# Optimization experiments

Hardware: AMD Instinct MI355X
Metric: run time of the kernel (lower is better)

The kernel has to match this reference:

```python
import jax, jax.numpy as jnp
import numpy as np

DIM = 768  # N, feature length and Linear dim
B, C = 16, 1024  # batch, token count


def setup_inputs() -> dict:
    key = jax.random.key(0)
    ks = jax.random.split(key, 7)
    s = 1.0 / np.sqrt(DIM)
    return {
        "x": jax.random.normal(ks[0], (B, C, DIM), dtype=jnp.float32),
        "Wq": jax.random.uniform(ks[1], (DIM, DIM), jnp.float32, -s, s),
        "bq": jax.random.uniform(ks[2], (DIM,), jnp.float32, -s, s),
        "Wk": jax.random.uniform(ks[3], (DIM, DIM), jnp.float32, -s, s),
        "bk": jax.random.uniform(ks[4], (DIM,), jnp.float32, -s, s),
        "Wv": jax.random.uniform(ks[5], (DIM, DIM), jnp.float32, -s, s),
        "bv": jax.random.uniform(ks[6], (DIM,), jnp.float32, -s, s),
    }


def reference(x, Wq, bq, Wk, bk, Wv, bv):
    # x: [B, C, N] with N == DIM; Linears act on last axis (torch y = x W^T + b)
    Bb, Cc, N = x.shape
    q = jnp.einsum("bcn,dn->bcd", x, Wq) + bq
    k = jnp.einsum("bcn,dn->bcd", x, Wk) + bk
    v = jnp.einsum("bcn,dn->bcd", x, Wv) + bv
    attn = jax.nn.softmax(jnp.einsum("bcd,bed->bce", q, k) * (N ** -0.5), axis=-1)  # [B,C,C]
    out = jnp.einsum("bce,ben->bcn", attn, v)  # [B,C,N]
    # faithful to torch: transpose(1,2) then reshape back to (B,C,N) -- a buffer reinterpretation
    out = jnp.transpose(out, (0, 2, 1)).reshape(Bb, Cc, N)
    return out + x  # dropout is identity at inference
```

## Files before the change

kernel.cpp:

```cpp
#include <hip/hip_runtime.h>
#include <hip/hip_bf16.h>

typedef __bf16 v8bf __attribute__((ext_vector_type(8)));
typedef float f32x4 __attribute__((ext_vector_type(4)));

static __device__ __forceinline__ unsigned short f2b(float f){
  union { float f; unsigned int u; } c; c.f = f;
  return (unsigned short)((c.u + 0x7FFFu + ((c.u >> 16) & 1u)) >> 16);
}
static __device__ __forceinline__ float b2f(unsigned int h){
  union { unsigned int u; float f; } c; c.u = h << 16; return c.f;
}

static __device__ __forceinline__ void gld_lds16(const void* g, void* l){
  __builtin_amdgcn_global_load_lds(
      (const __attribute__((address_space(1))) unsigned int*)g,
      (__attribute__((address_space(3))) unsigned int*)l, 16, 0, 0);
}

template<int NW, bool PREF>
static __device__ __forceinline__ void gemm256(
    const unsigned short* __restrict__ A, int lda,
    const unsigned short* __restrict__ B, int ldb,
    int NT, unsigned short* smem, f32x4 acc[8][NW])
{
  const int tid  = threadIdx.x;
  const int lane = tid & 63;
  const int w    = tid >> 6;
  const int wr   = w >> 2, wc = w & 3;
  const int lr   = lane & 15, lg = lane >> 4;
  char* sm = (char*)smem;

  #pragma unroll
  for (int m=0;m<8;++m)
    #pragma unroll
    for (int n=0;n<NW;++n)
      acc[m][n] = (f32x4){0.f,0.f,0.f,0.f};

  const int rloc = tid >> 3;
  const int scol = ((tid & 7) ^ ((tid >> 3) & 7)) << 3;
  const unsigned short* Ab0 = A + (size_t)rloc*lda + scol;
  const unsigned short* Bb0 = B + (size_t)rloc*ldb + scol;

  auto stA = [&](int ds, int i, int kE){
    gld_lds16(Ab0 + (size_t)(i*64)*lda + kE, sm + ds*32768 + i*8192 + w*1024);
  };
  auto stB = [&](int ds, int i, int kE){
    gld_lds16(Bb0 + (size_t)(i*64)*ldb + kE, sm + 65536 + ds*(NW*8192) + i*8192 + w*1024);
  };

  #pragma unroll
  for (int i=0;i<4;++i)  stA(0,i,0);
  #pragma unroll
  for (int i=0;i<NW;++i) stB(0,i,0);
  #pragma unroll
  for (int i=0;i<NW;++i) stB(1,i,64);
  if (NW==4) asm volatile("s_waitcnt vmcnt(4)" ::: "memory");
  else       asm volatile("s_waitcnt vmcnt(3)" ::: "memory");
  __builtin_amdgcn_s_barrier();

  const int ce0 = (((lg*8))      ^ ((lr&7)<<3)) * 2;
  const int ce1 = (((32 + lg*8)) ^ ((lr&7)<<3)) * 2;

  for (int kt = 0; kt < NT; ++kt) {
    const int d  = kt & 1;
    char* Abase = sm + d*32768 + wr*16384;
    char* Bbase = sm + 65536 + d*(NW*8192) + wc*(NW*2048);
    const int kA = (kt+1 < NT ? kt+1 : NT-1)*64;
    const int kB = (kt+2 < NT ? kt+2 : NT-1)*64;
    v8bf bfr[NW][2], af0[2][2], af1[2][2];

    auto rdA = [&](v8bf (&dst)[2][2], int qq){
      #pragma unroll
      for (int mm=0;mm<2;++mm){
        char* rp = Abase + ((qq*2+mm)*16+lr)*128;
        dst[mm][0] = *(const v8bf*)(rp + ce0);
        dst[mm][1] = *(const v8bf*)(rp + ce1);
      }
    };
    auto domfma = [&](v8bf (&cur)[2][2], int qq){
      #pragma unroll
      for (int mm=0;mm<2;++mm)
        #pragma unroll
        for (int n=0;n<NW;++n){
          acc[qq*2+mm][n] = __builtin_amdgcn_mfma_f32_16x16x32_bf16(cur[mm][0], bfr[n][0], acc[qq*2+mm][n], 0,0,0);
          acc[qq*2+mm][n] = __builtin_amdgcn_mfma_f32_16x16x32_bf16(cur[mm][1], bfr[n][1], acc[qq*2+mm][n], 0,0,0);
        }
    };

    #pragma unroll
    for (int q=0;q<4;++q) {
      if (q==0) {
        #pragma unroll
        for (int n=0;n<NW;++n){
          char* rp = Bbase + (n*16+lr)*128;
          bfr[n][0] = *(const v8bf*)(rp + ce0);
          bfr[n][1] = *(const v8bf*)(rp + ce1);
        }
        rdA(af0, 0);
      } else if (!PREF) {
        if ((q&1)==0) rdA(af0, q); else rdA(af1, q);
      }
      if      (q==0){ stA(d^1,0,kA); stA(d^1,1,kA); }
      else if (q==1){ stA(d^1,2,kA); stA(d^1,3,kA); }
      else if (q==2){ stB(d,0,kB);   stB(d,1,kB);   }
      else {
        #pragma unroll
        for (int i=2;i<NW;++i) stB(d,i,kB);
      }
      __builtin_amdgcn_s_barrier();
      asm volatile("s_waitcnt lgkmcnt(0)" ::: "memory");
      __builtin_amdgcn_sched_barrier(0);
      if (PREF && q<3) { if ((q&1)==0) rdA(af1, q+1); else rdA(af0, q+1); }
      __builtin_amdgcn_s_setprio(1);
      if ((q&1)==0) domfma(af0, q); else domfma(af1, q);
      __builtin_amdgcn_s_setprio(0);
      if (q==3){
        if (NW==4) asm volatile("s_waitcnt vmcnt(4)" ::: "memory");
        else       asm volatile("s_waitcnt vmcnt(3)" ::: "memory");
      }
      __builtin_amdgcn_s_barrier();
    }
  }
}

__global__ __launch_bounds__(256) void convert_kernel(
    const float* __restrict__ x,
    const float* __restrict__ Wq, const float* __restrict__ Wk,
    const float* __restrict__ Wv,
    unsigned short* __restrict__ Xb, unsigned short* __restrict__ Wb)
{
  const int NX = 3145728;
  const int NW_ = 147456;
  const int total = NX + 3*NW_;
  for (int i = blockIdx.x*256 + threadIdx.x; i < total; i += gridDim.x*256) {
    const float* src; unsigned short* dst; int off;
    if (i < NX) { src = x; dst = Xb; off = i; }
    else {
      int j = i - NX; int z = j / NW_; off = j - z*NW_;
      src = (z==0) ? Wq : ((z==1) ? Wk : Wv);
      dst = Wb + (size_t)z*589824;
    }
    float4 v = reinterpret_cast<const float4*>(src)[off];
    ushort4 h; h.x=f2b(v.x); h.y=f2b(v.y); h.z=f2b(v.z); h.w=f2b(v.w);
    reinterpret_cast<ushort4*>(dst)[off] = h;
  }
}

__global__ __launch_bounds__(512, 2) void qkv_kernel(
    const unsigned short* __restrict__ Xb, const unsigned short* __restrict__ Wb,
    const float* __restrict__ bq, const float* __restrict__ bk,
    const float* __restrict__ bv,
    unsigned short* __restrict__ Qb, unsigned short* __restrict__ Kb,
    unsigned short* __restrict__ Vt)
{
  extern __shared__ unsigned short smem[];
  const int bid = blockIdx.x;
  const int wg  = (bid & 7)*96 + (bid >> 3);
  const int mt  = wg / 12, nt = wg % 12;

  f32x4 acc[8][3];
  gemm256<3,true>(Xb + (size_t)mt*256*768, 768,
                  Wb + (size_t)nt*192*768, 768, 12, smem, acc);

  const int tid = threadIdx.x, lane = tid & 63, w = tid >> 6;
  const int wr = w >> 2, wc = w & 3, lr = lane & 15, lg = lane >> 4;
  const int z = nt >> 2;
  const float* bias = (z==0) ? bq : ((z==1) ? bk : bv);
  const int colbase = (nt & 3)*192 + wc*48;

  if (z < 2) {
    unsigned short* dst = (z==0) ? Qb : Kb;
    #pragma unroll
    for (int m=0;m<8;++m){
      int row0 = mt*256 + wr*128 + m*16 + lg*4;
      #pragma unroll
      for (int n=0;n<3;++n){
        int col = colbase + n*16 + lr;
        float bb = bias[col];
        #pragma unroll
        for (int r=0;r<4;++r)
          dst[(size_t)(row0+r)*768 + col] = f2b(acc[m][n][r] + bb);
      }
    }
  } else {
    const int rowG0 = mt*256;
    const int batch = rowG0 >> 10;
    const int ebase = rowG0 & 1023;
    unsigned short* dst = Vt + (size_t)batch*786432;
    #pragma unroll
    for (int m=0;m<8;++m){
      int e0 = ebase + wr*128 + m*16 + lg*4;
      #pragma unroll
      for (int n=0;n<3;++n){
        int col = colbase + n*16 + lr;
        float bb = bias[col];
        ushort4 h;
        h.x = f2b(acc[m][n][0] + bb);
        h.y = f2b(acc[m][n][1] + bb);
        h.z = f2b(acc[m][n][2] + bb);
        h.w = f2b(acc[m][n][3] + bb);
        *reinterpret_cast<ushort4*>(dst + (size_t)col*1024 + e0) = h;
      }
    }
  }
}

__global__ __launch_bounds__(512, 2) void scores_kernel(
    const unsigned short* __restrict__ Qb,
    const unsigned short* __restrict__ Kb,
    unsigned short* __restrict__ Sb)
{
  extern __shared__ unsigned short smem[];
  const int mt = blockIdx.x, nt = blockIdx.y, b = blockIdx.z;

  f32x4 acc[8][4];
  gemm256<4,false>(Qb + (size_t)b*786432 + (size_t)mt*256*768, 768,
                   Kb + (size_t)b*786432 + (size_t)nt*256*768, 768, 12, smem, acc);

  const float scale = 0.03608439182435161f;
  const int tid = threadIdx.x, lane = tid & 63, w = tid >> 6;
  const int wr = w >> 2, wc = w & 3, lr = lane & 15, lg = lane >> 4;
  unsigned short* dst = Sb + (size_t)b*1048576;
  #pragma unroll
  for (int m=0;m<8;++m){
    int row0 = mt*256 + wr*128 + m*16 + lg*4;
    #pragma unroll
    for (int n=0;n<4;++n){
      int col = nt*256 + wc*64 + n*16 + lr;
      #pragma unroll
      for (int r=0;r<4;++r)
        dst[(size_t)(row0+r)*1024 + col] = f2b(acc[m][n][r] * scale);
    }
  }
}

__global__ __launch_bounds__(256) void softmax_kernel(unsigned short* __restrict__ S)
{
  int row  = blockIdx.x*4 + (threadIdx.x >> 6);
  int lane = threadIdx.x & 63;
  unsigned short* p = S + (size_t)row*1024 + lane*16;
  uint4 v0 = *reinterpret_cast<const uint4*>(p);
  uint4 v1 = *reinterpret_cast<const uint4*>(p + 8);
  unsigned int uu[8] = {v0.x, v0.y, v0.z, v0.w, v1.x, v1.y, v1.z, v1.w};
  float f[16];
  #pragma unroll
  for (int i=0;i<8;++i){ f[2*i] = b2f(uu[i] & 0xffffu); f[2*i+1] = b2f(uu[i] >> 16); }

  float mx = -1e30f;
  #pragma unroll
  for (int i=0;i<16;++i) mx = fmaxf(mx, f[i]);
  #pragma unroll
  for (int off=1; off<64; off<<=1) mx = fmaxf(mx, __shfl_xor(mx, off, 64));

  float s = 0.f;
  #pragma unroll
  for (int i=0;i<16;++i){ f[i] = __expf(f[i] - mx); s += f[i]; }
  #pragma unroll
  for (int off=1; off<64; off<<=1) s += __shfl_xor(s, off, 64);
  float inv = 1.0f / s;

  #pragma unroll
  for (int i=0;i<8;++i){
    unsigned int lo = f2b(f[2*i] * inv);
    unsigned int hi = f2b(f[2*i+1] * inv);
    uu[i] = lo | (hi << 16);
  }
  uint4 o0; o0.x=uu[0]; o0.y=uu[1]; o0.z=uu[2]; o0.w=uu[3];
  uint4 o1; o1.x=uu[4]; o1.y=uu[5]; o1.z=uu[6]; o1.w=uu[7];
  *reinterpret_cast<uint4*>(p)     = o0;
  *reinterpret_cast<uint4*>(p + 8) = o1;
}

__global__ __launch_bounds__(512, 2) void pv_kernel(
    const unsigned short* __restrict__ P,
    const unsigned short* __restrict__ Vt,
    const float* __restrict__ x, float* __restrict__ out)
{
  extern __shared__ unsigned short smem[];
  const int mt = blockIdx.x, nt = blockIdx.y, b = blockIdx.z;

  f32x4 acc[8][3];
  gemm256<3,true>(P  + (size_t)b*1048576 + (size_t)mt*256*1024, 1024,
                  Vt + (size_t)b*786432  + (size_t)nt*192*1024, 1024, 16, smem, acc);

  const int tid = threadIdx.x, lane = tid & 63, w = tid >> 6;
  const int wr = w >> 2, wc = w & 3, lr = lane & 15, lg = lane >> 4;
  const float* xb = x   + (size_t)b*786432;
  float*       ob = out + (size_t)b*786432;
  #pragma unroll
  for (int m=0;m<8;++m){
    int c0 = mt*256 + wr*128 + m*16 + lg*4;
    #pragma unroll
    for (int n=0;n<3;++n){
      int col = nt*192 + wc*48 + n*16 + lr;
      size_t idx = (size_t)col*1024 + c0;
      float4 xv = *reinterpret_cast<const float4*>(xb + idx);
      float4 o;
      o.x = acc[m][n][0] + xv.x;
      o.y = acc[m][n][1] + xv.y;
      o.z = acc[m][n][2] + xv.z;
      o.w = acc[m][n][3] + xv.w;
      *reinterpret_cast<float4*>(ob + idx) = o;
    }
  }
}

extern "C" void kernel_launch(void* const* d_in, const int* in_sizes, int n_in,
                              void* d_out, int out_size, void* d_ws, size_t ws_size,
                              hipStream_t stream)
{
  const float* x  = (const float*)d_in[0];
  const float* Wq = (const float*)d_in[1];
  const float* bq = (const float*)d_in[2];
  const float* Wk = (const float*)d_in[3];
  const float* bk = (const float*)d_in[4];
  const float* Wv = (const float*)d_in[5];
  const float* bv = (const float*)d_in[6];
  float* out = (float*)d_out;

  char* ws = (char*)d_ws;
  unsigned short* Xb = (unsigned short*)(ws);
  unsigned short* Wb = (unsigned short*)(ws + 25165824);
  unsigned short* Sb = (unsigned short*)(ws);
  unsigned short* Qb = (unsigned short*)(ws + 33554432);
  unsigned short* Kb = (unsigned short*)(ws + 58720256);
  unsigned short* Vt = (unsigned short*)(ws + 83886080);

  convert_kernel<<<dim3(2048),     dim3(256), 0, stream>>>(x, Wq, Wk, Wv, Xb, Wb);
  qkv_kernel    <<<dim3(768),      dim3(512), 114688, stream>>>(Xb, Wb, bq, bk, bv, Qb, Kb, Vt);
  scores_kernel <<<dim3(4, 4, 16), dim3(512), 131072, stream>>>(Qb, Kb, Sb);
  softmax_kernel<<<dim3(4096),     dim3(256), 0, stream>>>(Sb);
  pv_kernel     <<<dim3(4, 4, 16), dim3(512), 114688, stream>>>(Sb, Vt, x, out);
}
```

Measured before the change: 173.1 us.

## Software-pipeline LDS fragment reads across MFMA phases in QKV and PV GEMMs

```diff
diff --git a/kernel.cpp b/kernel.cpp
--- a/kernel.cpp
+++ b/kernel.cpp
@@ -18,8 +18,10 @@
       (__attribute__((address_space(3))) unsigned int*)l, 16, 0, 0);
 }
 
-template<int NW, bool PREF>
-static __device__ __forceinline__ void gemm256(
+#define FENCE __builtin_amdgcn_sched_barrier(0)
+
+template<int NW>
+static __device__ __forceinline__ void gemm256p(
     const unsigned short* __restrict__ A, int lda,
     const unsigned short* __restrict__ B, int ldb,
     int NT, unsigned short* smem, f32x4 acc[8][NW])
@@ -49,14 +51,130 @@
     gld_lds16(Bb0 + (size_t)(i*64)*ldb + kE, sm + 65536 + ds*(NW*8192) + i*8192 + w*1024);
   };
 
+  const int ce0 = (((lg*8))      ^ ((lr&7)<<3)) * 2;
+  const int ce1 = (((32 + lg*8)) ^ ((lr&7)<<3)) * 2;
+
+  v8bf bX[NW][2], bY[NW][2], af0[2][2], af1[2][2];
+
+  auto rdA = [&](v8bf (&dst)[2][2], char* base, int qq){
+    #pragma unroll
+    for (int mm=0;mm<2;++mm){
+      char* rp = base + ((qq*2+mm)*16+lr)*128;
+      dst[mm][0] = *(const v8bf*)(rp + ce0);
+      dst[mm][1] = *(const v8bf*)(rp + ce1);
+    }
+  };
+  auto rdB = [&](v8bf (&dst)[NW][2], char* base){
+    #pragma unroll
+    for (int n=0;n<NW;++n){
+      char* rp = base + (n*16+lr)*128;
+      dst[n][0] = *(const v8bf*)(rp + ce0);
+      dst[n][1] = *(const v8bf*)(rp + ce1);
+    }
+  };
+  auto domfma = [&](v8bf (&a)[2][2], v8bf (&bb)[NW][2], int qq){
+    __builtin_amdgcn_s_setprio(1);
+    #pragma unroll
+    for (int mm=0;mm<2;++mm)
+      #pragma unroll
+      for (int n=0;n<NW;++n){
+        acc[qq*2+mm][n] = __builtin_amdgcn_mfma_f32_16x16x32_bf16(a[mm][0], bb[n][0], acc[qq*2+mm][n], 0,0,0);
+        acc[qq*2+mm][n] = __builtin_amdgcn_mfma_f32_16x16x32_bf16(a[mm][1], bb[n][1], acc[qq*2+mm][n], 0,0,0);
+      }
+    __builtin_amdgcn_s_setprio(0);
+  };
+
+  auto ktile = [&](int kt, int d, v8bf (&bc)[NW][2], v8bf (&bn)[NW][2]){
+    char* Ab = sm + d*32768 + wr*16384;
+    char* An = sm + (d^1)*32768 + wr*16384;
+    char* Bn = sm + 65536 + (d^1)*(NW*8192) + wc*(NW*2048);
+    const int kA = (kt+1 < NT ? kt+1 : NT-1)*64;
+    const int kB = (kt+2 < NT ? kt+2 : NT-1)*64;
+
+    stA(d^1,0,kA); stA(d^1,1,kA);
+    rdA(af1, Ab, 1);
+    FENCE; asm volatile("s_waitcnt lgkmcnt(4)" ::: "memory"); FENCE;
+    domfma(af0, bc, 0);
+    __builtin_amdgcn_s_barrier();
+
+    stA(d^1,2,kA); stA(d^1,3,kA);
+    rdA(af0, Ab, 2);
+    FENCE; asm volatile("s_waitcnt lgkmcnt(4)" ::: "memory"); FENCE;
+    domfma(af1, bc, 1);
+    __builtin_amdgcn_s_barrier();
+
+    stB(d,0,kB); stB(d,1,kB);
+    rdA(af1, Ab, 3);
+    FENCE; asm volatile("s_waitcnt lgkmcnt(4)" ::: "memory"); FENCE;
+    domfma(af0, bc, 2);
+    asm volatile("s_waitcnt vmcnt(2)" ::: "memory");
+    __builtin_amdgcn_s_barrier();
+
+    #pragma unroll
+    for (int i=2;i<NW;++i) stB(d,i,kB);
+    rdA(af0, An, 0);
+    rdB(bn, Bn);
+    if (NW==3) { FENCE; asm volatile("s_waitcnt lgkmcnt(10)" ::: "memory"); FENCE; }
+    else       { FENCE; asm volatile("s_waitcnt lgkmcnt(12)" ::: "memory"); FENCE; }
+    domfma(af1, bc, 3);
+    __builtin_amdgcn_s_barrier();
+  };
+
   #pragma unroll
   for (int i=0;i<4;++i)  stA(0,i,0);
   #pragma unroll
   for (int i=0;i<NW;++i) stB(0,i,0);
   #pragma unroll
   for (int i=0;i<NW;++i) stB(1,i,64);
-  if (NW==4) asm volatile("s_waitcnt vmcnt(4)" ::: "memory");
-  else       asm volatile("s_waitcnt vmcnt(3)" ::: "memory");
+  if (NW==3) asm volatile("s_waitcnt vmcnt(3)" ::: "memory");
+  else       asm volatile("s_waitcnt vmcnt(4)" ::: "memory");
+  __builtin_amdgcn_s_barrier();
+  rdB(bX, sm + 65536 + wc*(NW*2048));
+  rdA(af0, sm + wr*16384, 0);
+
+  for (int kt = 0; kt < NT; kt += 2) {
+    ktile(kt,   0, bX, bY);
+    ktile(kt+1, 1, bY, bX);
+  }
+}
+
+static __device__ __forceinline__ void gemm256v1(
+    const unsigned short* __restrict__ A, int lda,
+    const unsigned short* __restrict__ B, int ldb,
+    int NT, unsigned short* smem, f32x4 acc[8][4])
+{
+  const int tid  = threadIdx.x;
+  const int lane = tid & 63;
+  const int w    = tid >> 6;
+  const int wr   = w >> 2, wc = w & 3;
+  const int lr   = lane & 15, lg = lane >> 4;
+  char* sm = (char*)smem;
+
+  #pragma unroll
+  for (int m=0;m<8;++m)
+    #pragma unroll
+    for (int n=0;n<4;++n)
+      acc[m][n] = (f32x4){0.f,0.f,0.f,0.f};
+
+  const int rloc = tid >> 3;
+  const int scol = ((tid & 7) ^ ((tid >> 3) & 7)) << 3;
+  const unsigned short* Ab0 = A + (size_t)rloc*lda + scol;
+  const unsigned short* Bb0 = B + (size_t)rloc*ldb + scol;
+
+  auto stA = [&](int ds, int i, int kE){
+    gld_lds16(Ab0 + (size_t)(i*64)*lda + kE, sm + ds*32768 + i*8192 + w*1024);
+  };
+  auto stB = [&](int ds, int i, int kE){
+    gld_lds16(Bb0 + (size_t)(i*64)*ldb + kE, sm + 65536 + ds*32768 + i*8192 + w*1024);
+  };
+
+  #pragma unroll
+  for (int i=0;i<4;++i) stA(0,i,0);
+  #pragma unroll
+  for (int i=0;i<4;++i) stB(0,i,0);
+  #pragma unroll
+  for (int i=0;i<4;++i) stB(1,i,64);
+  asm volatile("s_waitcnt vmcnt(4)" ::: "memory");
   __builtin_amdgcn_s_barrier();
 
   const int ce0 = (((lg*8))      ^ ((lr&7)<<3)) * 2;
@@ -65,10 +183,10 @@
   for (int kt = 0; kt < NT; ++kt) {
     const int d  = kt & 1;
     char* Abase = sm + d*32768 + wr*16384;
-    char* Bbase = sm + 65536 + d*(NW*8192) + wc*(NW*2048);
+    char* Bbase = sm + 65536 + d*32768 + wc*8192;
     const int kA = (kt+1 < NT ? kt+1 : NT-1)*64;
     const int kB = (kt+2 < NT ? kt+2 : NT-1)*64;
-    v8bf bfr[NW][2], af0[2][2], af1[2][2];
+    v8bf bfr[4][2], af0[2][2], af1[2][2];
 
     auto rdA = [&](v8bf (&dst)[2][2], int qq){
       #pragma unroll
@@ -82,7 +200,7 @@
       #pragma unroll
       for (int mm=0;mm<2;++mm)
         #pragma unroll
-        for (int n=0;n<NW;++n){
+        for (int n=0;n<4;++n){
           acc[qq*2+mm][n] = __builtin_amdgcn_mfma_f32_16x16x32_bf16(cur[mm][0], bfr[n][0], acc[qq*2+mm][n], 0,0,0);
           acc[qq*2+mm][n] = __builtin_amdgcn_mfma_f32_16x16x32_bf16(cur[mm][1], bfr[n][1], acc[qq*2+mm][n], 0,0,0);
         }
@@ -92,33 +210,26 @@
     for (int q=0;q<4;++q) {
       if (q==0) {
         #pragma unroll
-        for (int n=0;n<NW;++n){
+        for (int n=0;n<4;++n){
           char* rp = Bbase + (n*16+lr)*128;
           bfr[n][0] = *(const v8bf*)(rp + ce0);
           bfr[n][1] = *(const v8bf*)(rp + ce1);
         }
         rdA(af0, 0);
-      } else if (!PREF) {
+      } else {
         if ((q&1)==0) rdA(af0, q); else rdA(af1, q);
       }
       if      (q==0){ stA(d^1,0,kA); stA(d^1,1,kA); }
       else if (q==1){ stA(d^1,2,kA); stA(d^1,3,kA); }
       else if (q==2){ stB(d,0,kB);   stB(d,1,kB);   }
-      else {
-        #pragma unroll
-        for (int i=2;i<NW;++i) stB(d,i,kB);
-      }
+      else          { stB(d,2,kB);   stB(d,3,kB);   }
       __builtin_amdgcn_s_barrier();
       asm volatile("s_waitcnt lgkmcnt(0)" ::: "memory");
-      __builtin_amdgcn_sched_barrier(0);
-      if (PREF && q<3) { if ((q&1)==0) rdA(af1, q+1); else rdA(af0, q+1); }
+      FENCE;
       __builtin_amdgcn_s_setprio(1);
       if ((q&1)==0) domfma(af0, q); else domfma(af1, q);
       __builtin_amdgcn_s_setprio(0);
-      if (q==3){
-        if (NW==4) asm volatile("s_waitcnt vmcnt(4)" ::: "memory");
-        else       asm volatile("s_waitcnt vmcnt(3)" ::: "memory");
-      }
+      if (q==3) asm volatile("s_waitcnt vmcnt(4)" ::: "memory");
       __builtin_amdgcn_s_barrier();
     }
   }
@@ -160,8 +271,8 @@
   const int mt  = wg / 12, nt = wg % 12;
 
   f32x4 acc[8][3];
-  gemm256<3,true>(Xb + (size_t)mt*256*768, 768,
-                  Wb + (size_t)nt*192*768, 768, 12, smem, acc);
+  gemm256p<3>(Xb + (size_t)mt*256*768, 768,
+              Wb + (size_t)nt*192*768, 768, 12, smem, acc);
 
   const int tid = threadIdx.x, lane = tid & 63, w = tid >> 6;
   const int wr = w >> 2, wc = w & 3, lr = lane & 15, lg = lane >> 4;
@@ -215,8 +326,8 @@
   const int mt = blockIdx.x, nt = blockIdx.y, b = blockIdx.z;
 
   f32x4 acc[8][4];
-  gemm256<4,false>(Qb + (size_t)b*786432 + (size_t)mt*256*768, 768,
-                   Kb + (size_t)b*786432 + (size_t)nt*256*768, 768, 12, smem, acc);
+  gemm256v1(Qb + (size_t)b*786432 + (size_t)mt*256*768, 768,
+            Kb + (size_t)b*786432 + (size_t)nt*256*768, 768, 12, smem, acc);
 
   const float scale = 0.03608439182435161f;
   const int tid = threadIdx.x, lane = tid & 63, w = tid >> 6;
@@ -281,8 +392,8 @@
   const int mt = blockIdx.x, nt = blockIdx.y, b = blockIdx.z;
 
   f32x4 acc[8][3];
-  gemm256<3,true>(P  + (size_t)b*1048576 + (size_t)mt*256*1024, 1024,
-                  Vt + (size_t)b*786432  + (size_t)nt*192*1024, 1024, 16, smem, acc);
+  gemm256p<3>(P  + (size_t)b*1048576 + (size_t)mt*256*1024, 1024,
+              Vt + (size_t)b*786432  + (size_t)nt*192*1024, 1024, 16, smem, acc);
 
   const int tid = threadIdx.x, lane = tid & 63, w = tid >> 6;
   const int wr = w >> 2, wc = w & 3, lr = lane & 15, lg = lane >> 4;
```

Measured after the change: 165.1 us. -4.6%, faster.

## Fold softmax into score epilogue and PV normalization, deepen GEMM pipelining

Applied to the files above, without the earlier changes.

```diff
diff --git a/kernel.cpp b/kernel.cpp
--- a/kernel.cpp
+++ b/kernel.cpp
@@ -10,6 +10,13 @@
 }
 static __device__ __forceinline__ float b2f(unsigned int h){
   union { unsigned int u; float f; } c; c.u = h << 16; return c.f;
+}
+static __device__ __forceinline__ float sum8(v8bf v){
+  union { v8bf v; unsigned int u[4]; } c; c.v = v;
+  float s = 0.f;
+  #pragma unroll
+  for (int i=0;i<4;++i){ s += b2f(c.u[i] & 0xffffu); s += b2f(c.u[i] >> 16); }
+  return s;
 }
 
 static __device__ __forceinline__ void gld_lds16(const void* g, void* l){
@@ -18,11 +25,13 @@
       (__attribute__((address_space(3))) unsigned int*)l, 16, 0, 0);
 }
 
-template<int NW, bool PREF>
-static __device__ __forceinline__ void gemm256(
+#define FENCE __builtin_amdgcn_sched_barrier(0)
+
+template<int NW, bool DEEP, bool RS>
+static __device__ __forceinline__ void gemmcore(
     const unsigned short* __restrict__ A, int lda,
     const unsigned short* __restrict__ B, int ldb,
-    int NT, unsigned short* smem, f32x4 acc[8][NW])
+    int NT, unsigned short* smem, f32x4 acc[8][NW], float* rs)
 {
   const int tid  = threadIdx.x;
   const int lane = tid & 63;
@@ -30,96 +39,139 @@
   const int wr   = w >> 2, wc = w & 3;
   const int lr   = lane & 15, lg = lane >> 4;
   char* sm = (char*)smem;
+  constexpr int NAB   = DEEP ? 3 : 2;
+  constexpr int BBASE = NAB * 32768;
+  constexpr int BBUF  = NW * 8192;
 
   #pragma unroll
   for (int m=0;m<8;++m)
     #pragma unroll
     for (int n=0;n<NW;++n)
       acc[m][n] = (f32x4){0.f,0.f,0.f,0.f};
+  if (RS) {
+    #pragma unroll
+    for (int m=0;m<8;++m) rs[m] = 0.f;
+  }
 
   const int rloc = tid >> 3;
   const int scol = ((tid & 7) ^ ((tid >> 3) & 7)) << 3;
   const unsigned short* Ab0 = A + (size_t)rloc*lda + scol;
   const unsigned short* Bb0 = B + (size_t)rloc*ldb + scol;
 
-  auto stA = [&](int ds, int i, int kE){
-    gld_lds16(Ab0 + (size_t)(i*64)*lda + kE, sm + ds*32768 + i*8192 + w*1024);
-  };
-  auto stB = [&](int ds, int i, int kE){
-    gld_lds16(Bb0 + (size_t)(i*64)*ldb + kE, sm + 65536 + ds*(NW*8192) + i*8192 + w*1024);
-  };
-
-  #pragma unroll
-  for (int i=0;i<4;++i)  stA(0,i,0);
-  #pragma unroll
-  for (int i=0;i<NW;++i) stB(0,i,0);
-  #pragma unroll
-  for (int i=0;i<NW;++i) stB(1,i,64);
-  if (NW==4) asm volatile("s_waitcnt vmcnt(4)" ::: "memory");
-  else       asm volatile("s_waitcnt vmcnt(3)" ::: "memory");
-  __builtin_amdgcn_s_barrier();
+  auto stA = [&](int ab, int i, int kE){
+    gld_lds16(Ab0 + (size_t)(i*64)*lda + kE, sm + ab*32768 + i*8192 + w*1024);
+  };
+  auto stB = [&](int db, int i, int kE){
+    gld_lds16(Bb0 + (size_t)(i*64)*ldb + kE, sm + BBASE + db*BBUF + i*8192 + w*1024);
+  };
 
   const int ce0 = (((lg*8))      ^ ((lr&7)<<3)) * 2;
   const int ce1 = (((32 + lg*8)) ^ ((lr&7)<<3)) * 2;
 
-  for (int kt = 0; kt < NT; ++kt) {
-    const int d  = kt & 1;
-    char* Abase = sm + d*32768 + wr*16384;
-    char* Bbase = sm + 65536 + d*(NW*8192) + wc*(NW*2048);
-    const int kA = (kt+1 < NT ? kt+1 : NT-1)*64;
+  v8bf bX[NW][2], bY[NW][2], af0[2][2], af1[2][2];
+
+  auto rdA = [&](v8bf (&dst)[2][2], char* base, int qq){
+    #pragma unroll
+    for (int mm=0;mm<2;++mm){
+      char* rp = base + ((qq*2+mm)*16+lr)*128;
+      dst[mm][0] = *(const v8bf*)(rp + ce0);
+      dst[mm][1] = *(const v8bf*)(rp + ce1);
+    }
+  };
+  auto rdB = [&](v8bf (&dst)[NW][2], char* base){
+    #pragma unroll
+    for (int n=0;n<NW;++n){
+      char* rp = base + (n*16+lr)*128;
+      dst[n][0] = *(const v8bf*)(rp + ce0);
+      dst[n][1] = *(const v8bf*)(rp + ce1);
+    }
+  };
+  auto domfma = [&](v8bf (&a)[2][2], v8bf (&bb)[NW][2], int qq){
+    __builtin_amdgcn_s_setprio(1);
+    #pragma unroll
+    for (int mm=0;mm<2;++mm)
+      #pragma unroll
+      for (int n=0;n<NW;++n){
+        acc[qq*2+mm][n] = __builtin_amdgcn_mfma_f32_16x16x32_bf16(a[mm][0], bb[n][0], acc[qq*2+mm][n], 0,0,0);
+        acc[qq*2+mm][n] = __builtin_amdgcn_mfma_f32_16x16x32_bf16(a[mm][1], bb[n][1], acc[qq*2+mm][n], 0,0,0);
+      }
+    __builtin_amdgcn_s_setprio(0);
+    if (RS){
+      rs[qq*2]   += sum8(a[0][0]) + sum8(a[0][1]);
+      rs[qq*2+1] += sum8(a[1][0]) + sum8(a[1][1]);
+    }
+  };
+
+  auto ktile = [&](int kt, int ar, int an, int as,
+                   v8bf (&bc)[NW][2], v8bf (&bn)[NW][2]){
+    char* Ab = sm + ar*32768 + wr*16384;
+    char* An = sm + an*32768 + wr*16384;
+    char* Bn = sm + BBASE + ((kt+1)&1)*BBUF + wc*(NW*2048);
+    const int kAraw = DEEP ? kt+2 : kt+1;
+    const int kA = (kAraw < NT ? kAraw : NT-1)*64;
     const int kB = (kt+2 < NT ? kt+2 : NT-1)*64;
-    v8bf bfr[NW][2], af0[2][2], af1[2][2];
-
-    auto rdA = [&](v8bf (&dst)[2][2], int qq){
-      #pragma unroll
-      for (int mm=0;mm<2;++mm){
-        char* rp = Abase + ((qq*2+mm)*16+lr)*128;
-        dst[mm][0] = *(const v8bf*)(rp + ce0);
-        dst[mm][1] = *(const v8bf*)(rp + ce1);
-      }
-    };
-    auto domfma = [&](v8bf (&cur)[2][2], int qq){
-      #pragma unroll
-      for (int mm=0;mm<2;++mm)
-        #pragma unroll
-        for (int n=0;n<NW;++n){
-          acc[qq*2+mm][n] = __builtin_amdgcn_mfma_f32_16x16x32_bf16(cur[mm][0], bfr[n][0], acc[qq*2+mm][n], 0,0,0);
-          acc[qq*2+mm][n] = __builtin_amdgcn_mfma_f32_16x16x32_bf16(cur[mm][1], bfr[n][1], acc[qq*2+mm][n], 0,0,0);
-        }
-    };
-
-    #pragma unroll
-    for (int q=0;q<4;++q) {
-      if (q==0) {
-        #pragma unroll
-        for (int n=0;n<NW;++n){
-          char* rp = Bbase + (n*16+lr)*128;
-          bfr[n][0] = *(const v8bf*)(rp + ce0);
-          bfr[n][1] = *(const v8bf*)(rp + ce1);
-        }
-        rdA(af0, 0);
-      } else if (!PREF) {
-        if ((q&1)==0) rdA(af0, q); else rdA(af1, q);
-      }
-      if      (q==0){ stA(d^1,0,kA); stA(d^1,1,kA); }
-      else if (q==1){ stA(d^1,2,kA); stA(d^1,3,kA); }
-      else if (q==2){ stB(d,0,kB);   stB(d,1,kB);   }
-      else {
-        #pragma unroll
-        for (int i=2;i<NW;++i) stB(d,i,kB);
-      }
-      __builtin_amdgcn_s_barrier();
-      asm volatile("s_waitcnt lgkmcnt(0)" ::: "memory");
-      __builtin_amdgcn_sched_barrier(0);
-      if (PREF && q<3) { if ((q&1)==0) rdA(af1, q+1); else rdA(af0, q+1); }
-      __builtin_amdgcn_s_setprio(1);
-      if ((q&1)==0) domfma(af0, q); else domfma(af1, q);
-      __builtin_amdgcn_s_setprio(0);
-      if (q==3){
-        if (NW==4) asm volatile("s_waitcnt vmcnt(4)" ::: "memory");
-        else       asm volatile("s_waitcnt vmcnt(3)" ::: "memory");
-      }
-      __builtin_amdgcn_s_barrier();
+    const int db = kt & 1;
+
+    stA(as,0,kA); stA(as,1,kA);
+    rdA(af1, Ab, 1);
+    FENCE; asm volatile("s_waitcnt lgkmcnt(4)" ::: "memory"); FENCE;
+    domfma(af0, bc, 0);
+    __builtin_amdgcn_s_barrier();
+
+    stA(as,2,kA); stA(as,3,kA);
+    rdA(af0, Ab, 2);
+    FENCE; asm volatile("s_waitcnt lgkmcnt(4)" ::: "memory"); FENCE;
+    domfma(af1, bc, 1);
+    __builtin_amdgcn_s_barrier();
+
+    stB(db,0,kB); stB(db,1,kB);
+    rdA(af1, Ab, 3);
+    FENCE; asm volatile("s_waitcnt lgkmcnt(4)" ::: "memory"); FENCE;
+    domfma(af0, bc, 2);
+    if constexpr (DEEP) asm volatile("s_waitcnt vmcnt(6)" ::: "memory");
+    else                asm volatile("s_waitcnt vmcnt(2)" ::: "memory");
+    __builtin_amdgcn_s_barrier();
+
+    #pragma unroll
+    for (int i=2;i<NW;++i) stB(db,i,kB);
+    rdA(af0, An, 0);
+    rdB(bn, Bn);
+    if constexpr (NW==3) { FENCE; asm volatile("s_waitcnt lgkmcnt(10)" ::: "memory"); FENCE; }
+    else                 { FENCE; asm volatile("s_waitcnt lgkmcnt(12)" ::: "memory"); FENCE; }
+    domfma(af1, bc, 3);
+    __builtin_amdgcn_s_barrier();
+  };
+
+  #pragma unroll
+  for (int i=0;i<4;++i)  stA(0,i,0);
+  #pragma unroll
+  for (int i=0;i<NW;++i) stB(0,i,0);
+  if constexpr (DEEP) {
+    #pragma unroll
+    for (int i=0;i<4;++i) stA(1,i,64);
+  }
+  #pragma unroll
+  for (int i=0;i<NW;++i) stB(1,i,64);
+  if constexpr (DEEP)      asm volatile("s_waitcnt vmcnt(7)" ::: "memory");
+  else if constexpr (NW==3) asm volatile("s_waitcnt vmcnt(3)" ::: "memory");
+  else                      asm volatile("s_waitcnt vmcnt(4)" ::: "memory");
+  __builtin_amdgcn_s_barrier();
+  rdB(bX, sm + BBASE + wc*(NW*2048));
+  rdA(af0, sm + wr*16384, 0);
+
+  if constexpr (DEEP) {
+    int c0 = 0;
+    for (int kt = 0; kt < NT; kt += 2) {
+      const int c1 = (c0+1==3) ? 0 : c0+1;
+      const int c2 = (c1+1==3) ? 0 : c1+1;
+      ktile(kt,   c0, c1, c2, bX, bY);
+      ktile(kt+1, c1, c2, c0, bY, bX);
+      c0 = c2;
+    }
+  } else {
+    for (int kt = 0; kt < NT; kt += 2) {
+      ktile(kt,   0, 1, 1, bX, bY);
+      ktile(kt+1, 1, 0, 0, bY, bX);
     }
   }
 }
@@ -160,8 +212,8 @@
   const int mt  = wg / 12, nt = wg % 12;
 
   f32x4 acc[8][3];
-  gemm256<3,true>(Xb + (size_t)mt*256*768, 768,
-                  Wb + (size_t)nt*192*768, 768, 12, smem, acc);
+  gemmcore<3,true,false>(Xb + (size_t)mt*256*768, 768,
+                         Wb + (size_t)nt*192*768, 768, 12, smem, acc, nullptr);
 
   const int tid = threadIdx.x, lane = tid & 63, w = tid >> 6;
   const int wr = w >> 2, wc = w & 3, lr = lane & 15, lg = lane >> 4;
@@ -209,19 +261,20 @@
 __global__ __launch_bounds__(512, 2) void scores_kernel(
     const unsigned short* __restrict__ Qb,
     const unsigned short* __restrict__ Kb,
-    unsigned short* __restrict__ Sb)
+    unsigned short* __restrict__ Eb)
 {
   extern __shared__ unsigned short smem[];
   const int mt = blockIdx.x, nt = blockIdx.y, b = blockIdx.z;
 
   f32x4 acc[8][4];
-  gemm256<4,false>(Qb + (size_t)b*786432 + (size_t)mt*256*768, 768,
-                   Kb + (size_t)b*786432 + (size_t)nt*256*768, 768, 12, smem, acc);
+  gemmcore<4,false,false>(Qb + (size_t)b*786432 + (size_t)mt*256*768, 768,
+                          Kb + (size_t)b*786432 + (size_t)nt*256*768, 768,
+                          12, smem, acc, nullptr);
 
   const float scale = 0.03608439182435161f;
   const int tid = threadIdx.x, lane = tid & 63, w = tid >> 6;
   const int wr = w >> 2, wc = w & 3, lr = lane & 15, lg = lane >> 4;
-  unsigned short* dst = Sb + (size_t)b*1048576;
+  unsigned short* dst = Eb + (size_t)b*1048576;
   #pragma unroll
   for (int m=0;m<8;++m){
     int row0 = mt*256 + wr*128 + m*16 + lg*4;
@@ -230,50 +283,13 @@
       int col = nt*256 + wc*64 + n*16 + lr;
       #pragma unroll
       for (int r=0;r<4;++r)
-        dst[(size_t)(row0+r)*1024 + col] = f2b(acc[m][n][r] * scale);
-    }
-  }
-}
-
-__global__ __launch_bounds__(256) void softmax_kernel(unsigned short* __restrict__ S)
-{
-  int row  = blockIdx.x*4 + (threadIdx.x >> 6);
-  int lane = threadIdx.x & 63;
-  unsigned short* p = S + (size_t)row*1024 + lane*16;
-  uint4 v0 = *reinterpret_cast<const uint4*>(p);
-  uint4 v1 = *reinterpret_cast<const uint4*>(p + 8);
-  unsigned int uu[8] = {v0.x, v0.y, v0.z, v0.w, v1.x, v1.y, v1.z, v1.w};
-  float f[16];
-  #pragma unroll
-  for (int i=0;i<8;++i){ f[2*i] = b2f(uu[i] & 0xffffu); f[2*i+1] = b2f(uu[i] >> 16); }
-
-  float mx = -1e30f;
-  #pragma unroll
-  for (int i=0;i<16;++i) mx = fmaxf(mx, f[i]);
-  #pragma unroll
-  for (int off=1; off<64; off<<=1) mx = fmaxf(mx, __shfl_xor(mx, off, 64));
-
-  float s = 0.f;
-  #pragma unroll
-  for (int i=0;i<16;++i){ f[i] = __expf(f[i] - mx); s += f[i]; }
-  #pragma unroll
-  for (int off=1; off<64; off<<=1) s += __shfl_xor(s, off, 64);
-  float inv = 1.0f / s;
-
-  #pragma unroll
-  for (int i=0;i<8;++i){
-    unsigned int lo = f2b(f[2*i] * inv);
-    unsigned int hi = f2b(f[2*i+1] * inv);
-    uu[i] = lo | (hi << 16);
-  }
-  uint4 o0; o0.x=uu[0]; o0.y=uu[1]; o0.z=uu[2]; o0.w=uu[3];
-  uint4 o1; o1.x=uu[4]; o1.y=uu[5]; o1.z=uu[6]; o1.w=uu[7];
-  *reinterpret_cast<uint4*>(p)     = o0;
-  *reinterpret_cast<uint4*>(p + 8) = o1;
+        dst[(size_t)(row0+r)*1024 + col] = f2b(__expf(acc[m][n][r] * scale));
+    }
+  }
 }
 
 __global__ __launch_bounds__(512, 2) void pv_kernel(
-    const unsigned short* __restrict__ P,
+    const unsigned short* __restrict__ Eb,
     const unsigned short* __restrict__ Vt,
     const float* __restrict__ x, float* __restrict__ out)
 {
@@ -281,26 +297,39 @@
   const int mt = blockIdx.x, nt = blockIdx.y, b = blockIdx.z;
 
   f32x4 acc[8][3];
-  gemm256<3,true>(P  + (size_t)b*1048576 + (size_t)mt*256*1024, 1024,
-                  Vt + (size_t)b*786432  + (size_t)nt*192*1024, 1024, 16, smem, acc);
+  float rs[8];
+  gemmcore<3,true,true>(Eb + (size_t)b*1048576 + (size_t)mt*256*1024, 1024,
+                        Vt + (size_t)b*786432  + (size_t)nt*192*1024, 1024,
+                        16, smem, acc, rs);
 
   const int tid = threadIdx.x, lane = tid & 63, w = tid >> 6;
   const int wr = w >> 2, wc = w & 3, lr = lane & 15, lg = lane >> 4;
+
+  #pragma unroll
+  for (int m=0;m<8;++m){
+    rs[m] += __shfl_xor(rs[m], 16, 64);
+    rs[m] += __shfl_xor(rs[m], 32, 64);
+  }
+
   const float* xb = x   + (size_t)b*786432;
   float*       ob = out + (size_t)b*786432;
   #pragma unroll
   for (int m=0;m<8;++m){
     int c0 = mt*256 + wr*128 + m*16 + lg*4;
+    float inv0 = 1.0f / __shfl(rs[m], lg*4 + 0, 64);
+    float inv1 = 1.0f / __shfl(rs[m], lg*4 + 1, 64);
+    float inv2 = 1.0f / __shfl(rs[m], lg*4 + 2, 64);
+    float inv3 = 1.0f / __shfl(rs[m], lg*4 + 3, 64);
     #pragma unroll
     for (int n=0;n<3;++n){
       int col = nt*192 + wc*48 + n*16 + lr;
       size_t idx = (size_t)col*1024 + c0;
       float4 xv = *reinterpret_cast<const float4*>(xb + idx);
       float4 o;
-      o.x = acc[m][n][0] + xv.x;
-      o.y = acc[m][n][1] + xv.y;
-      o.z = acc[m][n][2] + xv.z;
-      o.w = acc[m][n][3] + xv.w;
+      o.x = acc[m][n][0]*inv0 + xv.x;
+      o.y = acc[m][n][1]*inv1 + xv.y;
+      o.z = acc[m][n][2]*inv2 + xv.z;
+      o.w = acc[m][n][3]*inv3 + xv.w;
       *reinterpret_cast<float4*>(ob + idx) = o;
     }
   }
@@ -322,14 +351,13 @@
   char* ws = (char*)d_ws;
   unsigned short* Xb = (unsigned short*)(ws);
   unsigned short* Wb = (unsigned short*)(ws + 25165824);
-  unsigned short* Sb = (unsigned short*)(ws);
+  unsigned short* Eb = (unsigned short*)(ws);
   unsigned short* Qb = (unsigned short*)(ws + 33554432);
   unsigned short* Kb = (unsigned short*)(ws + 58720256);
   unsigned short* Vt = (unsigned short*)(ws + 83886080);
 
-  convert_kernel<<<dim3(2048),     dim3(256), 0, stream>>>(x, Wq, Wk, Wv, Xb, Wb);
-  qkv_kernel    <<<dim3(768),      dim3(512), 114688, stream>>>(Xb, Wb, bq, bk, bv, Qb, Kb, Vt);
-  scores_kernel <<<dim3(4, 4, 16), dim3(512), 131072, stream>>>(Qb, Kb, Sb);
-  softmax_kernel<<<dim3(4096),     dim3(256), 0, stream>>>(Sb);
-  pv_kernel     <<<dim3(4, 4, 16), dim3(512), 114688, stream>>>(Sb, Vt, x, out);
-}
+  convert_kernel<<<dim3(2048),     dim3(256), 0,      stream>>>(x, Wq, Wk, Wv, Xb, Wb);
+  qkv_kernel    <<<dim3(768),      dim3(512), 147456, stream>>>(Xb, Wb, bq, bk, bv, Qb, Kb, Vt);
+  scores_kernel <<<dim3(4, 4, 16), dim3(512), 131072, stream>>>(Qb, Kb, Eb);
+  pv_kernel     <<<dim3(4, 4, 16), dim3(512), 147456, stream>>>(Eb, Vt, x, out);
+}
```

Result: slower. 239.0 us (+38.1%).
